# Performance work log

Hardware: AMD Instinct MI355X
Metric: run time of the kernel (lower is better)

Reference implementation:

```python
import jax, jax.numpy as jnp
import numpy as np

N = 50000          # nodes
E = 800000         # edges per metapath
M = 3              # metapaths
IN_DIM = 256
H = 8              # heads
D = 32             # out_dim per head
HID = 128          # semantic attention hidden
NEG_SLOPE = 0.2    # DGL GATConv default leaky_relu slope


def setup_inputs() -> dict:
    key = jax.random.key(0)
    ks = jax.random.split(key, 10)
    h = jax.random.normal(ks[0], (N, IN_DIM), dtype=jnp.float32)
    src = jax.random.randint(ks[1], (M, E), 0, N, dtype=jnp.int32)
    dst = jax.random.randint(ks[2], (M, E), 0, N, dtype=jnp.int32)
    s = 1.0 / np.sqrt(IN_DIM)
    fc_w = jax.random.normal(ks[3], (M, IN_DIM, H * D), dtype=jnp.float32) * s
    attn_l = jax.random.normal(ks[4], (M, H, D), dtype=jnp.float32) * 0.1
    attn_r = jax.random.normal(ks[5], (M, H, D), dtype=jnp.float32) * 0.1
    bias = jnp.zeros((M, H * D), dtype=jnp.float32)
    sem_w1 = jax.random.normal(ks[6], (H * D, HID), dtype=jnp.float32) * (1.0 / np.sqrt(H * D))
    sem_b1 = jnp.zeros((HID,), dtype=jnp.float32)
    sem_w2 = jax.random.normal(ks[7], (HID, 1), dtype=jnp.float32) * (1.0 / np.sqrt(HID))
    return {"h": h, "src": src, "dst": dst, "fc_w": fc_w, "attn_l": attn_l,
            "attn_r": attn_r, "bias": bias, "sem_w1": sem_w1, "sem_b1": sem_b1,
            "sem_w2": sem_w2}


def _gat(h, src, dst, fc_w, attn_l, attn_r, bias):
    # DGL GATConv (eval mode, dropout=0), activation=elu.
    feat = (h @ fc_w).reshape(N, H, D)                       # [N,H,D]
    el = jnp.sum(feat * attn_l, axis=-1)                     # [N,H]
    er = jnp.sum(feat * attn_r, axis=-1)                     # [N,H]
    e = jax.nn.leaky_relu(el[src] + er[dst], NEG_SLOPE)      # [E,H]
    # edge softmax over incoming edges of each dst node
    emax = jax.ops.segment_max(e, dst, num_segments=N)       # [N,H]
    emax = jnp.where(jnp.isfinite(emax), emax, 0.0)
    ee = jnp.exp(e - emax[dst])                              # [E,H]
    esum = jax.ops.segment_sum(ee, dst, num_segments=N)      # [N,H]
    alpha = ee / jnp.maximum(esum[dst], 1e-38)               # [E,H]
    msg = feat[src] * alpha[:, :, None]                      # [E,H,D]
    rst = jax.ops.segment_sum(msg, dst, num_segments=N)      # [N,H,D]
    rst = rst + bias.reshape(1, H, D)
    return jax.nn.elu(rst).reshape(N, H * D)                 # flatten heads


def reference(h, src, dst, fc_w, attn_l, attn_r, bias, sem_w1, sem_b1, sem_w2):
    gat_all = jax.vmap(_gat, in_axes=(None, 0, 0, 0, 0, 0, 0))
    z_m = gat_all(h, src, dst, fc_w, attn_l, attn_r, bias)   # [M,N,F]
    z_m = jnp.transpose(z_m, (1, 0, 2))                      # [N,M,F]
    # semantic attention
    w = jnp.tanh(z_m @ sem_w1 + sem_b1) @ sem_w2             # [N,M,1]
    w = w.mean(axis=0)                                       # [M,1]
    a_w = jax.nn.softmax(w, axis=0)                          # [M,1]
    z = jnp.sum(z_m * a_w[None, :, :], axis=1)               # [N,F]
    return z
```

## Files before the change

kernel.cpp:

```cpp
#include <hip/hip_runtime.h>
#include <math.h>

#define NN   50000
#define EE   800000
#define MM   3
#define KDIM 256
#define FF   256
#define HH   8
#define DD   32
#define HID  128
#define SLOPE 0.2f
#define BK   32
#define CAP  80

typedef unsigned short u16;
typedef unsigned int   u32;
typedef __attribute__((ext_vector_type(8))) short short8;
typedef __attribute__((ext_vector_type(4))) float floatx4;

__device__ __forceinline__ float eluf(float x) { return x > 0.f ? x : expm1f(x); }

__device__ __forceinline__ float b2f_lo(u32 u) {
    union { u32 i; float f; } v; v.i = u << 16; return v.f;
}
__device__ __forceinline__ float b2f_hi(u32 u) {
    union { u32 i; float f; } v; v.i = u & 0xffff0000u; return v.f;
}
__device__ __forceinline__ u16 f2b(float f) {
    union { float f; u32 i; } v; v.f = f;
    u32 lsb = (v.i >> 16) & 1u;
    v.i += 0x7fffu + lsb;
    return (u16)(v.i >> 16);
}
__device__ __forceinline__ u32 pack2(float lo, float hi) {
    return (u32)f2b(lo) | ((u32)f2b(hi) << 16);
}

__device__ __forceinline__ void gload_lds16(const u16* g, u16* l) {
    __builtin_amdgcn_global_load_lds(
        (const __attribute__((address_space(1))) unsigned int*)(const void*)g,
        (__attribute__((address_space(3))) unsigned int*)(void*)l,
        16, 0, 0);
}

__global__ __launch_bounds__(256) void k_cast_h(
    const float* __restrict__ hmat, u16* __restrict__ hb)
{
    long long i = ((long long)blockIdx.x * 256 + threadIdx.x) * 8;
    if (i >= (long long)NN * KDIM) return;
    float4 v0 = *(const float4*)(hmat + i);
    float4 v1 = *(const float4*)(hmat + i + 4);
    uint4 u;
    u.x = pack2(v0.x, v0.y); u.y = pack2(v0.z, v0.w);
    u.z = pack2(v1.x, v1.y); u.w = pack2(v1.z, v1.w);
    *(uint4*)(hb + i) = u;
}

__global__ __launch_bounds__(256) void k_cast_w(
    const float* __restrict__ fcw, u16* __restrict__ fcwt)
{
    int k = blockIdx.x, m = blockIdx.y, n = threadIdx.x;
    float v = fcw[((size_t)m * KDIM + k) * FF + n];
    fcwt[((size_t)m * FF + n) * KDIM + k] = f2b(v);
}

__global__ __launch_bounds__(128) void k_cast_w1(
    const float* __restrict__ w1, u16* __restrict__ w1t)
{
    int k = blockIdx.x, n = threadIdx.x;
    w1t[(size_t)n * KDIM + k] = f2b(w1[(size_t)k * HID + n]);
}

__global__ __launch_bounds__(256) void k_feat_all(
    const u16*   __restrict__ hb,
    const u16*   __restrict__ fcwt,
    const float* __restrict__ al,
    const float* __restrict__ ar,
    u16*   __restrict__ featb,
    float* __restrict__ el,
    float* __restrict__ er,
    const int* __restrict__ src,
    const int* __restrict__ dst,
    int* __restrict__ cnt,
    u16* __restrict__ srt)
{
    __shared__ u16 As[128 * BK];
    __shared__ u16 Bs[128 * BK];

    const int t = threadIdx.x;

    {
        int bid = blockIdx.x + 391 * (blockIdx.y + 2 * blockIdx.z);
        long long base = ((long long)bid * 256 + t) * 4;
        if (base < (long long)MM * EE) {
            int4 d4 = *(const int4*)(dst + base);
            int4 s4 = *(const int4*)(src + base);
            int me = (int)(base / EE);
            int* cnt_m = cnt + (size_t)me * NN;
            u16* srt_m = srt + (size_t)me * CAP * NN;
            int dd4[4] = { d4.x, d4.y, d4.z, d4.w };
            int ss4[4] = { s4.x, s4.y, s4.z, s4.w };
            #pragma unroll
            for (int j = 0; j < 4; ++j) {
                int slot = atomicAdd(&cnt_m[dd4[j]], 1);
                if (slot < CAP) srt_m[(size_t)slot * NN + dd4[j]] = (u16)ss4[j];
            }
        }
    }

    const int n0 = blockIdx.x * 128;
    const int cy = blockIdx.y;
    const int m  = blockIdx.z;
    const int c_base = cy * 128;
    const int wave = t >> 6, lane = t & 63;
    const int wr = wave >> 1, wc = wave & 1;
    const int quad = lane >> 4, l15 = lane & 15;

    const u16* fcwt_m = fcwt + (size_t)m * FF * KDIM;
    const float* al_m = al + (size_t)m * HH * DD;
    const float* ar_m = ar + (size_t)m * HH * DD;

    const u16* pA[2]; const u16* pB[2]; u16* lA[2]; u16* lB[2];
    #pragma unroll
    for (int i = 0; i < 2; ++i) {
        int r  = wave * 32 + i * 16 + (lane >> 2);
        int cs = (((lane & 3) ^ (r & 3)) << 3);
        pA[i] = hb + (size_t)min(n0 + r, NN - 1) * KDIM + cs;
        pB[i] = fcwt_m + (size_t)(c_base + r) * KDIM + cs;
        lA[i] = (u16*)As + (wave * 2 + i) * 512;
        lB[i] = (u16*)Bs + (wave * 2 + i) * 512;
    }

    int aoff[4], boff[4];
    #pragma unroll
    for (int ti = 0; ti < 4; ++ti) {
        int rowa = wr * 64 + ti * 16 + l15;
        aoff[ti] = rowa * BK + (((quad ^ (rowa & 3))) << 3);
        int rowb = wc * 64 + ti * 16 + l15;
        boff[ti] = rowb * BK + (((quad ^ (rowb & 3))) << 3);
    }

    floatx4 acc[4][4] = {};

    for (int k0 = 0; k0 < KDIM; k0 += BK) {
        __syncthreads();
        #pragma unroll
        for (int i = 0; i < 2; ++i) {
            gload_lds16(pA[i] + k0, lA[i]);
            gload_lds16(pB[i] + k0, lB[i]);
        }
        __syncthreads();

        short8 afr[4], bfr[4];
        #pragma unroll
        for (int ti = 0; ti < 4; ++ti)
            afr[ti] = *(const short8*)(&As[aoff[ti]]);
        #pragma unroll
        for (int tj = 0; tj < 4; ++tj)
            bfr[tj] = *(const short8*)(&Bs[boff[tj]]);
        #pragma unroll
        for (int ti = 0; ti < 4; ++ti)
            #pragma unroll
            for (int tj = 0; tj < 4; ++tj)
                acc[ti][tj] = __builtin_amdgcn_mfma_f32_16x16x32_bf16(
                    afr[ti], bfr[tj], acc[ti][tj], 0, 0, 0);
    }

    float alv[4], arv[4];
    #pragma unroll
    for (int tj = 0; tj < 4; ++tj) {
        int h = cy * 4 + wc * 2 + (tj >> 1);
        int dcol = (tj & 1) * 16 + l15;
        alv[tj] = al_m[h * DD + dcol];
        arv[tj] = ar_m[h * DD + dcol];
    }
    const int h0 = cy * 4 + wc * 2, h1 = h0 + 1;

    #pragma unroll
    for (int ti = 0; ti < 4; ++ti) {
        #pragma unroll
        for (int reg = 0; reg < 4; ++reg) {
            int n = n0 + wr * 64 + ti * 16 + quad * 4 + reg;
            bool ok = n < NN;
            if (ok) {
                #pragma unroll
                for (int tj = 0; tj < 4; ++tj) {
                    int c = c_base + wc * 64 + tj * 16 + l15;
                    featb[((size_t)m * NN + n) * FF + c] = f2b(acc[ti][tj][reg]);
                }
            }
            float pl0 = acc[ti][0][reg] * alv[0] + acc[ti][1][reg] * alv[1];
            float pl1 = acc[ti][2][reg] * alv[2] + acc[ti][3][reg] * alv[3];
            float pr0 = acc[ti][0][reg] * arv[0] + acc[ti][1][reg] * arv[1];
            float pr1 = acc[ti][2][reg] * arv[2] + acc[ti][3][reg] * arv[3];
            #pragma unroll
            for (int s = 1; s < 16; s <<= 1) {
                pl0 += __shfl_xor(pl0, s); pl1 += __shfl_xor(pl1, s);
                pr0 += __shfl_xor(pr0, s); pr1 += __shfl_xor(pr1, s);
            }
            if (l15 == 0 && ok) {
                el[((size_t)m * NN + n) * HH + h0] = pl0;
                el[((size_t)m * NN + n) * HH + h1] = pl1;
                er[((size_t)m * NN + n) * HH + h0] = pr0;
                er[((size_t)m * NN + n) * HH + h1] = pr1;
            }
        }
    }
}

__global__ __launch_bounds__(256) void k_aggr_all(
    const int* __restrict__ cnt,
    const u16* __restrict__ srt,
    const float* __restrict__ el,
    const float* __restrict__ er,
    const u16* __restrict__ featb,
    const float* __restrict__ bias,
    u16* __restrict__ z,
    int m)
{
    __shared__ float alpha_s[4][2][CAP][HH];
    __shared__ int   srcoff[4][2][CAP];

    const int wave = threadIdx.x >> 6, lane = threadIdx.x & 63;
    const int half = lane >> 5, L = lane & 31;
    const int d = blockIdx.x * 8 + wave * 2 + half;

    const int deg = min(cnt[(size_t)m * NN + d], CAP);
    const float* el_m = el + (size_t)m * NN * HH;
    const u16* feat_m = featb + (size_t)m * NN * FF;

    #pragma unroll
    for (int i = 0; i < 3; ++i) {
        int slot = L + i * 32;
        if (slot < deg)
            srcoff[wave][half][slot] =
                (int)srt[(size_t)(m * CAP + slot) * NN + d] * FF;
    }

    const int hA = L & 7;
    const float er_d = er[((size_t)m * NN + d) * HH + hA];
    float esum_r = 0.f;
    const int nIter = (deg + 3) >> 2;
    int i = 0;
    for (; i + 2 <= nIter; i += 2) {
        int j0 = i * 4 + (L >> 3);
        int j1 = j0 + 4;
        bool v0 = j0 < deg, v1 = j1 < deg;
        int so0 = v0 ? srcoff[wave][half][j0] : 0;
        int so1 = v1 ? srcoff[wave][half][j1] : 0;
        float x0 = el_m[(size_t)(so0 >> 5) + hA] + er_d;
        float x1 = el_m[(size_t)(so1 >> 5) + hA] + er_d;
        x0 = x0 >= 0.f ? x0 : SLOPE * x0;  x0 = fminf(x0, 60.f);
        x1 = x1 >= 0.f ? x1 : SLOPE * x1;  x1 = fminf(x1, 60.f);
        float e0 = v0 ? expf(x0) : 0.f;
        float e1 = v1 ? expf(x1) : 0.f;
        if (v0) alpha_s[wave][half][j0][hA] = e0;
        if (v1) alpha_s[wave][half][j1][hA] = e1;
        float g = e0 + e1;
        g += __shfl_xor(g, 8); g += __shfl_xor(g, 16);
        esum_r += g;
    }
    for (; i < nIter; ++i) {
        int j = i * 4 + (L >> 3);
        float e = 0.f;
        if (j < deg) {
            int so = srcoff[wave][half][j];
            float x = el_m[(size_t)(so >> 5) + hA] + er_d;
            x = x >= 0.f ? x : SLOPE * x;
            x = fminf(x, 60.f);
            e = expf(x);
            alpha_s[wave][half][j][hA] = e;
        }
        float g = e;
        g += __shfl_xor(g, 8); g += __shfl_xor(g, 16);
        esum_r += g;
    }
    float inv_r = 1.f / fmaxf(esum_r, 1e-38f);

    const float inv_g = __shfl(inv_r, (lane & 32) | (L >> 2));
    const int hB = L >> 2;
    const u16* frow = feat_m + L * 8;
    float acc[8] = {0.f, 0.f, 0.f, 0.f, 0.f, 0.f, 0.f, 0.f};

#define ACC8(f, a)                                                  \
    acc[0] += (a) * b2f_lo((f).x); acc[1] += (a) * b2f_hi((f).x);   \
    acc[2] += (a) * b2f_lo((f).y); acc[3] += (a) * b2f_hi((f).y);   \
    acc[4] += (a) * b2f_lo((f).z); acc[5] += (a) * b2f_hi((f).z);   \
    acc[6] += (a) * b2f_lo((f).w); acc[7] += (a) * b2f_hi((f).w);

    int j = 0;
    for (; j + 4 <= deg; j += 4) {
        int so0 = srcoff[wave][half][j + 0];
        int so1 = srcoff[wave][half][j + 1];
        int so2 = srcoff[wave][half][j + 2];
        int so3 = srcoff[wave][half][j + 3];
        float a0 = alpha_s[wave][half][j + 0][hB];
        float a1 = alpha_s[wave][half][j + 1][hB];
        float a2 = alpha_s[wave][half][j + 2][hB];
        float a3 = alpha_s[wave][half][j + 3][hB];
        uint4 f0 = *(const uint4*)(frow + so0);
        uint4 f1 = *(const uint4*)(frow + so1);
        uint4 f2 = *(const uint4*)(frow + so2);
        uint4 f3 = *(const uint4*)(frow + so3);
        ACC8(f0, a0); ACC8(f1, a1); ACC8(f2, a2); ACC8(f3, a3);
    }
    for (; j < deg; ++j) {
        int so = srcoff[wave][half][j];
        float a = alpha_s[wave][half][j][hB];
        uint4 f = *(const uint4*)(frow + so);
        ACC8(f, a);
    }
#undef ACC8

    #pragma unroll
    for (int k = 0; k < 8; ++k) acc[k] *= inv_g;

    const float4 b0 = *(const float4*)(bias + (size_t)m * FF + L * 8);
    const float4 b1 = *(const float4*)(bias + (size_t)m * FF + L * 8 + 4);
    uint4 o;
    o.x = pack2(eluf(acc[0] + b0.x), eluf(acc[1] + b0.y));
    o.y = pack2(eluf(acc[2] + b0.z), eluf(acc[3] + b0.w));
    o.z = pack2(eluf(acc[4] + b1.x), eluf(acc[5] + b1.y));
    o.w = pack2(eluf(acc[6] + b1.z), eluf(acc[7] + b1.w));
    *(uint4*)(z + ((size_t)m * NN + d) * FF + L * 8) = o;
}

__global__ __launch_bounds__(256) void k_sem_all(
    const u16* __restrict__ z,
    const u16* __restrict__ w1t,
    const float* __restrict__ b1,
    const float* __restrict__ w2,
    float* __restrict__ wsum)
{
    __shared__ u16 As[128 * BK];
    __shared__ u16 Bs[128 * BK];

    const int n0 = blockIdx.x * 128;
    const int m  = blockIdx.y;
    const int t = threadIdx.x;
    const int wave = t >> 6, lane = t & 63;
    const int wr = wave >> 1, wc = wave & 1;
    const int quad = lane >> 4, l15 = lane & 15;

    const u16* z_m = z + (size_t)m * NN * FF;

    const u16* pA[2]; const u16* pB[2]; u16* lA[2]; u16* lB[2];
    #pragma unroll
    for (int i = 0; i < 2; ++i) {
        int r  = wave * 32 + i * 16 + (lane >> 2);
        int cs = (((lane & 3) ^ (r & 3)) << 3);
        pA[i] = z_m + (size_t)min(n0 + r, NN - 1) * FF + cs;
        pB[i] = w1t + (size_t)r * KDIM + cs;
        lA[i] = (u16*)As + (wave * 2 + i) * 512;
        lB[i] = (u16*)Bs + (wave * 2 + i) * 512;
    }

    int aoff[4], boff[4];
    #pragma unroll
    for (int ti = 0; ti < 4; ++ti) {
        int rowa = wr * 64 + ti * 16 + l15;
        aoff[ti] = rowa * BK + (((quad ^ (rowa & 3))) << 3);
        int rowb = wc * 64 + ti * 16 + l15;
        boff[ti] = rowb * BK + (((quad ^ (rowb & 3))) << 3);
    }

    floatx4 acc[4][4] = {};

    for (int k0 = 0; k0 < KDIM; k0 += BK) {
        __syncthreads();
        #pragma unroll
        for (int i = 0; i < 2; ++i) {
            gload_lds16(pA[i] + k0, lA[i]);
            gload_lds16(pB[i] + k0, lB[i]);
        }
        __syncthreads();

        short8 afr[4], bfr[4];
        #pragma unroll
        for (int ti = 0; ti < 4; ++ti)
            afr[ti] = *(const short8*)(&As[aoff[ti]]);
        #pragma unroll
        for (int tj = 0; tj < 4; ++tj)
            bfr[tj] = *(const short8*)(&Bs[boff[tj]]);
        #pragma unroll
        for (int ti = 0; ti < 4; ++ti)
            #pragma unroll
            for (int tj = 0; tj < 4; ++tj)
                acc[ti][tj] = __builtin_amdgcn_mfma_f32_16x16x32_bf16(
                    afr[ti], bfr[tj], acc[ti][tj], 0, 0, 0);
    }

    float b1v[4], w2v[4];
    #pragma unroll
    for (int tj = 0; tj < 4; ++tj) {
        int c = wc * 64 + tj * 16 + l15;
        b1v[tj] = b1[c];
        w2v[tj] = w2[c];
    }
    float local = 0.f;
    #pragma unroll
    for (int ti = 0; ti < 4; ++ti) {
        #pragma unroll
        for (int reg = 0; reg < 4; ++reg) {
            int n = n0 + wr * 64 + ti * 16 + quad * 4 + reg;
            if (n < NN) {
                #pragma unroll
                for (int tj = 0; tj < 4; ++tj)
                    local += tanhf(acc[ti][tj][reg] + b1v[tj]) * w2v[tj];
            }
        }
    }
    #pragma unroll
    for (int s = 1; s < 64; s <<= 1) local += __shfl_xor(local, s);
    if (lane == 0) atomicAdd(&wsum[m], local);
}

__global__ __launch_bounds__(256) void k_combine(
    const u16* __restrict__ z, const float* __restrict__ wsum,
    float* __restrict__ out)
{
    float s0 = wsum[0] / (float)NN, s1 = wsum[1] / (float)NN, s2 = wsum[2] / (float)NN;
    float mx = fmaxf(s0, fmaxf(s1, s2));
    float e0 = expf(s0 - mx), e1 = expf(s1 - mx), e2 = expf(s2 - mx);
    float inv = 1.f / (e0 + e1 + e2);
    float aw[3] = { e0 * inv, e1 * inv, e2 * inv };

    long long idx = (long long)blockIdx.x * 256 + threadIdx.x;
    if (idx >= (long long)NN * 32) return;
    int n = (int)(idx >> 5), c = (int)(idx & 31) * 8;
    float acc[8] = {0.f, 0.f, 0.f, 0.f, 0.f, 0.f, 0.f, 0.f};
    #pragma unroll
    for (int m = 0; m < MM; ++m) {
        uint4 f = *(const uint4*)(z + ((size_t)m * NN + n) * FF + c);
        float a = aw[m];
        acc[0] += a * b2f_lo(f.x); acc[1] += a * b2f_hi(f.x);
        acc[2] += a * b2f_lo(f.y); acc[3] += a * b2f_hi(f.y);
        acc[4] += a * b2f_lo(f.z); acc[5] += a * b2f_hi(f.z);
        acc[6] += a * b2f_lo(f.w); acc[7] += a * b2f_hi(f.w);
    }
    float* op = out + (size_t)n * FF + c;
    *(float4*)op       = make_float4(acc[0], acc[1], acc[2], acc[3]);
    *(float4*)(op + 4) = make_float4(acc[4], acc[5], acc[6], acc[7]);
}

extern "C" void kernel_launch(void* const* d_in, const int* in_sizes, int n_in,
                              void* d_out, int out_size, void* d_ws, size_t ws_size,
                              hipStream_t stream)
{
    const float* hmat = (const float*)d_in[0];
    const int*   src  = (const int*)d_in[1];
    const int*   dst  = (const int*)d_in[2];
    const float* fcw  = (const float*)d_in[3];
    const float* al   = (const float*)d_in[4];
    const float* ar   = (const float*)d_in[5];
    const float* bias = (const float*)d_in[6];
    const float* w1   = (const float*)d_in[7];
    const float* b1   = (const float*)d_in[8];
    const float* w2   = (const float*)d_in[9];
    float* out = (float*)d_out;

    char* ws = (char*)d_ws;
    size_t off = 0;
    auto alloc = [&](size_t nbytes) {
        void* p = (void*)(ws + off);
        off = (off + nbytes + 255) & ~(size_t)255;
        return p;
    };
    float* el   = (float*)alloc((size_t)MM * NN * HH * 4);
    float* er   = (float*)alloc((size_t)MM * NN * HH * 4);
    float* wsum = (float*)alloc(256);
    int*   cnt  = (int*)alloc((size_t)MM * NN * 4);
    u16*   srt  = (u16*)alloc((size_t)MM * CAP * NN * 2);
    u16*   fcwt = (u16*)alloc((size_t)MM * KDIM * FF * 2);
    u16*   w1t  = (u16*)alloc((size_t)HID * KDIM * 2);
    u16*   hb   = (u16*)alloc((size_t)NN * KDIM * 2);
    u16*   featb= (u16*)alloc((size_t)MM * NN * FF * 2);
    u16*   z    = (u16*)alloc((size_t)MM * NN * FF * 2);

    hipMemsetAsync(wsum, 0, 256, stream);
    hipMemsetAsync(cnt, 0, (size_t)MM * NN * 4, stream);

    k_cast_h<<<(int)(((size_t)NN * KDIM / 8 + 255) / 256), 256, 0, stream>>>(hmat, hb);
    k_cast_w<<<dim3(KDIM, MM), 256, 0, stream>>>(fcw, fcwt);
    k_cast_w1<<<KDIM, 128, 0, stream>>>(w1, w1t);

    k_feat_all<<<dim3((NN + 127) / 128, 2, MM), 256, 0, stream>>>(
        hb, fcwt, al, ar, featb, el, er, src, dst, cnt, srt);

    for (int m = 0; m < MM; ++m)
        k_aggr_all<<<NN / 8, 256, 0, stream>>>(
            cnt, srt, el, er, featb, bias, z, m);

    k_sem_all<<<dim3((NN + 127) / 128, MM), 256, 0, stream>>>(z, w1t, b1, w2, wsum);
    k_combine<<<(int)(((size_t)NN * 32 + 255) / 256), 256, 0, stream>>>(z, wsum, out);
}
```

Before: 569.2 us.

## Merge cast kernels with partial edge scatter; split feat and sem per metapath

The three cast kernels become one k_prep launch, which also scatters the first part of each metapath's edges into the per-destination buckets. The remaining edges are scattered inside per-metapath k_feat launches. The semantic GEMM is now launched per metapath right after that metapath's aggregation, so z for that metapath may still be in cache. This cuts launch count for the casts and spreads the atomic scatter work differently across kernels, at the cost of more launches for feat and sem, each with a smaller grid.

```diff
diff --git a/kernel.cpp b/kernel.cpp
--- a/kernel.cpp
+++ b/kernel.cpp
@@ -13,6 +13,15 @@
 #define BK   32
 #define CAP  80
 
+#define EPREP_BLK 272
+#define E_OFF     (EPREP_BLK * 1024)
+#define E_REST    (EE - E_OFF)
+#define PREP_SCAT (EPREP_BLK * MM)
+#define PREP_CH   6250
+#define PREP_CW   768
+#define PREP_CW1  128
+#define PREP_GRID (PREP_SCAT + PREP_CH + PREP_CW + PREP_CW1)
+
 typedef unsigned short u16;
 typedef unsigned int   u32;
 typedef __attribute__((ext_vector_type(8))) short short8;
@@ -43,35 +52,67 @@
         16, 0, 0);
 }
 
-__global__ __launch_bounds__(256) void k_cast_h(
-    const float* __restrict__ hmat, u16* __restrict__ hb)
-{
-    long long i = ((long long)blockIdx.x * 256 + threadIdx.x) * 8;
-    if (i >= (long long)NN * KDIM) return;
-    float4 v0 = *(const float4*)(hmat + i);
-    float4 v1 = *(const float4*)(hmat + i + 4);
-    uint4 u;
-    u.x = pack2(v0.x, v0.y); u.y = pack2(v0.z, v0.w);
-    u.z = pack2(v1.x, v1.y); u.w = pack2(v1.z, v1.w);
-    *(uint4*)(hb + i) = u;
-}
-
-__global__ __launch_bounds__(256) void k_cast_w(
-    const float* __restrict__ fcw, u16* __restrict__ fcwt)
-{
-    int k = blockIdx.x, m = blockIdx.y, n = threadIdx.x;
-    float v = fcw[((size_t)m * KDIM + k) * FF + n];
-    fcwt[((size_t)m * FF + n) * KDIM + k] = f2b(v);
-}
-
-__global__ __launch_bounds__(128) void k_cast_w1(
-    const float* __restrict__ w1, u16* __restrict__ w1t)
-{
-    int k = blockIdx.x, n = threadIdx.x;
-    w1t[(size_t)n * KDIM + k] = f2b(w1[(size_t)k * HID + n]);
-}
-
-__global__ __launch_bounds__(256) void k_feat_all(
+__device__ __forceinline__ void scat4(
+    const int* __restrict__ src, const int* __restrict__ dst,
+    int* __restrict__ cnt, u16* __restrict__ srt, int me, long long base)
+{
+    int4 d4 = *(const int4*)(dst + base);
+    int4 s4 = *(const int4*)(src + base);
+    int* cnt_m = cnt + (size_t)me * NN;
+    u16* srt_m = srt + (size_t)me * CAP * NN;
+    int dd4[4] = { d4.x, d4.y, d4.z, d4.w };
+    int ss4[4] = { s4.x, s4.y, s4.z, s4.w };
+    #pragma unroll
+    for (int j = 0; j < 4; ++j) {
+        int slot = atomicAdd(&cnt_m[dd4[j]], 1);
+        if (slot < CAP) srt_m[(size_t)slot * NN + dd4[j]] = (u16)ss4[j];
+    }
+}
+
+__global__ __launch_bounds__(256) void k_prep(
+    const float* __restrict__ hmat, u16* __restrict__ hb,
+    const float* __restrict__ fcw,  u16* __restrict__ fcwt,
+    const float* __restrict__ w1,   u16* __restrict__ w1t,
+    const int* __restrict__ src, const int* __restrict__ dst,
+    int* __restrict__ cnt, u16* __restrict__ srt)
+{
+    const int bid = blockIdx.x;
+    const int t = threadIdx.x;
+
+    if (bid < PREP_SCAT) {
+        int me = bid / EPREP_BLK, c = bid % EPREP_BLK;
+        long long base = (long long)me * EE + ((long long)c * 256 + t) * 4;
+        scat4(src, dst, cnt, srt, me, base);
+        return;
+    }
+    if (bid < PREP_SCAT + PREP_CH) {
+        long long i = (((long long)(bid - PREP_SCAT)) * 256 + t) * 8;
+        if (i < (long long)NN * KDIM) {
+            float4 v0 = *(const float4*)(hmat + i);
+            float4 v1 = *(const float4*)(hmat + i + 4);
+            uint4 u;
+            u.x = pack2(v0.x, v0.y); u.y = pack2(v0.z, v0.w);
+            u.z = pack2(v1.x, v1.y); u.w = pack2(v1.z, v1.w);
+            *(uint4*)(hb + i) = u;
+        }
+        return;
+    }
+    if (bid < PREP_SCAT + PREP_CH + PREP_CW) {
+        int wb = bid - PREP_SCAT - PREP_CH;
+        int k = wb & 255, me = wb >> 8, n = t;
+        float v = fcw[((size_t)me * KDIM + k) * FF + n];
+        fcwt[((size_t)me * FF + n) * KDIM + k] = f2b(v);
+        return;
+    }
+    {
+        int vb = bid - PREP_SCAT - PREP_CH - PREP_CW;
+        int idx = vb * 256 + t;
+        int k = idx >> 7, n = idx & 127;
+        w1t[(size_t)n * KDIM + k] = f2b(w1[(size_t)k * HID + n]);
+    }
+}
+
+__global__ __launch_bounds__(256) void k_feat(
     const u16*   __restrict__ hb,
     const u16*   __restrict__ fcwt,
     const float* __restrict__ al,
@@ -82,7 +123,8 @@
     const int* __restrict__ src,
     const int* __restrict__ dst,
     int* __restrict__ cnt,
-    u16* __restrict__ srt)
+    u16* __restrict__ srt,
+    int m)
 {
     __shared__ u16 As[128 * BK];
     __shared__ u16 Bs[128 * BK];
@@ -90,27 +132,14 @@
     const int t = threadIdx.x;
 
     {
-        int bid = blockIdx.x + 391 * (blockIdx.y + 2 * blockIdx.z);
-        long long base = ((long long)bid * 256 + t) * 4;
-        if (base < (long long)MM * EE) {
-            int4 d4 = *(const int4*)(dst + base);
-            int4 s4 = *(const int4*)(src + base);
-            int me = (int)(base / EE);
-            int* cnt_m = cnt + (size_t)me * NN;
-            u16* srt_m = srt + (size_t)me * CAP * NN;
-            int dd4[4] = { d4.x, d4.y, d4.z, d4.w };
-            int ss4[4] = { s4.x, s4.y, s4.z, s4.w };
-            #pragma unroll
-            for (int j = 0; j < 4; ++j) {
-                int slot = atomicAdd(&cnt_m[dd4[j]], 1);
-                if (slot < CAP) srt_m[(size_t)slot * NN + dd4[j]] = (u16)ss4[j];
-            }
-        }
+        int bf = blockIdx.x + 391 * blockIdx.y;
+        long long off = ((long long)bf * 256 + t) * 4;
+        if (off < E_REST)
+            scat4(src, dst, cnt, srt, m, (long long)m * EE + E_OFF + off);
     }
 
     const int n0 = blockIdx.x * 128;
     const int cy = blockIdx.y;
-    const int m  = blockIdx.z;
     const int c_base = cy * 128;
     const int wave = t >> 6, lane = t & 63;
     const int wr = wave >> 1, wc = wave & 1;
@@ -330,13 +359,13 @@
     const u16* __restrict__ w1t,
     const float* __restrict__ b1,
     const float* __restrict__ w2,
-    float* __restrict__ wsum)
+    float* __restrict__ wsum,
+    int m)
 {
     __shared__ u16 As[128 * BK];
     __shared__ u16 Bs[128 * BK];
 
     const int n0 = blockIdx.x * 128;
-    const int m  = blockIdx.y;
     const int t = threadIdx.x;
     const int wave = t >> 6, lane = t & 63;
     const int wr = wave >> 1, wc = wave & 1;
@@ -480,17 +509,18 @@
     hipMemsetAsync(wsum, 0, 256, stream);
     hipMemsetAsync(cnt, 0, (size_t)MM * NN * 4, stream);
 
-    k_cast_h<<<(int)(((size_t)NN * KDIM / 8 + 255) / 256), 256, 0, stream>>>(hmat, hb);
-    k_cast_w<<<dim3(KDIM, MM), 256, 0, stream>>>(fcw, fcwt);
-    k_cast_w1<<<KDIM, 128, 0, stream>>>(w1, w1t);
-
-    k_feat_all<<<dim3((NN + 127) / 128, 2, MM), 256, 0, stream>>>(
-        hb, fcwt, al, ar, featb, el, er, src, dst, cnt, srt);
+    k_prep<<<PREP_GRID, 256, 0, stream>>>(
+        hmat, hb, fcw, fcwt, w1, w1t, src, dst, cnt, srt);
 
     for (int m = 0; m < MM; ++m)
+        k_feat<<<dim3(391, 2), 256, 0, stream>>>(
+            hb, fcwt, al, ar, featb, el, er, src, dst, cnt, srt, m);
+
+    for (int m = 0; m < MM; ++m) {
         k_aggr_all<<<NN / 8, 256, 0, stream>>>(
             cnt, srt, el, er, featb, bias, z, m);
-
-    k_sem_all<<<dim3((NN + 127) / 128, MM), 256, 0, stream>>>(z, w1t, b1, w2, wsum);
+        k_sem_all<<<391, 256, 0, stream>>>(z, w1t, b1, w2, wsum, m);
+    }
+
     k_combine<<<(int)(((size_t)NN * 32 + 255) / 256), 256, 0, stream>>>(z, wsum, out);
 }
```

Result: slower. 635.3 us (+11.6%).

## Fuse h cast into GEMM loads, merge weight casts and per-metapath aggregation launches

Applied to the files above, without the earlier changes.

Removes the separate fp32-to-bf16 cast kernel for h: the GEMM now reads fp32 rows directly, converts them in registers and writes them to LDS, so the bf16 copy of h is never written to or read back from global memory. The two weight-cast kernels are merged into one launch, and the three per-metapath aggregation launches become a single 2D grid. In exchange, the A-tile load becomes a synchronous register round-trip instead of an async global-to-LDS load. h is also re-read and re-converted in fp32 by every column block and metapath (6 times).

```diff
diff --git a/kernel.cpp b/kernel.cpp
--- a/kernel.cpp
+++ b/kernel.cpp
@@ -43,36 +43,24 @@
         16, 0, 0);
 }
 
-__global__ __launch_bounds__(256) void k_cast_h(
-    const float* __restrict__ hmat, u16* __restrict__ hb)
-{
-    long long i = ((long long)blockIdx.x * 256 + threadIdx.x) * 8;
-    if (i >= (long long)NN * KDIM) return;
-    float4 v0 = *(const float4*)(hmat + i);
-    float4 v1 = *(const float4*)(hmat + i + 4);
-    uint4 u;
-    u.x = pack2(v0.x, v0.y); u.y = pack2(v0.z, v0.w);
-    u.z = pack2(v1.x, v1.y); u.w = pack2(v1.z, v1.w);
-    *(uint4*)(hb + i) = u;
-}
-
-__global__ __launch_bounds__(256) void k_cast_w(
-    const float* __restrict__ fcw, u16* __restrict__ fcwt)
-{
-    int k = blockIdx.x, m = blockIdx.y, n = threadIdx.x;
-    float v = fcw[((size_t)m * KDIM + k) * FF + n];
-    fcwt[((size_t)m * FF + n) * KDIM + k] = f2b(v);
-}
-
-__global__ __launch_bounds__(128) void k_cast_w1(
-    const float* __restrict__ w1, u16* __restrict__ w1t)
-{
-    int k = blockIdx.x, n = threadIdx.x;
-    w1t[(size_t)n * KDIM + k] = f2b(w1[(size_t)k * HID + n]);
+__global__ __launch_bounds__(256) void k_prep_w(
+    const float* __restrict__ fcw,  u16* __restrict__ fcwt,
+    const float* __restrict__ w1,   u16* __restrict__ w1t)
+{
+    const int bid = blockIdx.x;
+    if (bid < 768) {
+        int k = bid & 255, me = bid >> 8, n = threadIdx.x;
+        float v = fcw[((size_t)me * KDIM + k) * FF + n];
+        fcwt[((size_t)me * FF + n) * KDIM + k] = f2b(v);
+    } else {
+        int idx = (bid - 768) * 256 + threadIdx.x;
+        int k = idx >> 7, n = idx & 127;
+        w1t[(size_t)n * KDIM + k] = f2b(w1[(size_t)k * HID + n]);
+    }
 }
 
 __global__ __launch_bounds__(256) void k_feat_all(
-    const u16*   __restrict__ hb,
+    const float* __restrict__ hmat,
     const u16*   __restrict__ fcwt,
     const float* __restrict__ al,
     const float* __restrict__ ar,
@@ -120,14 +108,14 @@
     const float* al_m = al + (size_t)m * HH * DD;
     const float* ar_m = ar + (size_t)m * HH * DD;
 
-    const u16* pA[2]; const u16* pB[2]; u16* lA[2]; u16* lB[2];
+    const float* pAf[2]; const u16* pB[2]; u16* lA[2]; u16* lB[2];
     #pragma unroll
     for (int i = 0; i < 2; ++i) {
         int r  = wave * 32 + i * 16 + (lane >> 2);
         int cs = (((lane & 3) ^ (r & 3)) << 3);
-        pA[i] = hb + (size_t)min(n0 + r, NN - 1) * KDIM + cs;
-        pB[i] = fcwt_m + (size_t)(c_base + r) * KDIM + cs;
-        lA[i] = (u16*)As + (wave * 2 + i) * 512;
+        pAf[i] = hmat + (size_t)min(n0 + r, NN - 1) * KDIM + cs;
+        pB[i]  = fcwt_m + (size_t)(c_base + r) * KDIM + cs;
+        lA[i] = (u16*)As + (wave * 2 + i) * 512 + lane * 8;
         lB[i] = (u16*)Bs + (wave * 2 + i) * 512;
     }
 
@@ -145,9 +133,16 @@
     for (int k0 = 0; k0 < KDIM; k0 += BK) {
         __syncthreads();
         #pragma unroll
+        for (int i = 0; i < 2; ++i)
+            gload_lds16(pB[i] + k0, lB[i]);
+        #pragma unroll
         for (int i = 0; i < 2; ++i) {
-            gload_lds16(pA[i] + k0, lA[i]);
-            gload_lds16(pB[i] + k0, lB[i]);
+            float4 v0 = *(const float4*)(pAf[i] + k0);
+            float4 v1 = *(const float4*)(pAf[i] + k0 + 4);
+            uint4 u;
+            u.x = pack2(v0.x, v0.y); u.y = pack2(v0.z, v0.w);
+            u.z = pack2(v1.x, v1.y); u.w = pack2(v1.z, v1.w);
+            *(uint4*)(lA[i]) = u;
         }
         __syncthreads();
 
@@ -215,12 +210,12 @@
     const float* __restrict__ er,
     const u16* __restrict__ featb,
     const float* __restrict__ bias,
-    u16* __restrict__ z,
-    int m)
+    u16* __restrict__ z)
 {
     __shared__ float alpha_s[4][2][CAP][HH];
     __shared__ int   srcoff[4][2][CAP];
 
+    const int m = blockIdx.y;
     const int wave = threadIdx.x >> 6, lane = threadIdx.x & 63;
     const int half = lane >> 5, L = lane & 31;
     const int d = blockIdx.x * 8 + wave * 2 + half;
@@ -473,24 +468,19 @@
     u16*   srt  = (u16*)alloc((size_t)MM * CAP * NN * 2);
     u16*   fcwt = (u16*)alloc((size_t)MM * KDIM * FF * 2);
     u16*   w1t  = (u16*)alloc((size_t)HID * KDIM * 2);
-    u16*   hb   = (u16*)alloc((size_t)NN * KDIM * 2);
     u16*   featb= (u16*)alloc((size_t)MM * NN * FF * 2);
     u16*   z    = (u16*)alloc((size_t)MM * NN * FF * 2);
 
     hipMemsetAsync(wsum, 0, 256, stream);
     hipMemsetAsync(cnt, 0, (size_t)MM * NN * 4, stream);
 
-    k_cast_h<<<(int)(((size_t)NN * KDIM / 8 + 255) / 256), 256, 0, stream>>>(hmat, hb);
-    k_cast_w<<<dim3(KDIM, MM), 256, 0, stream>>>(fcw, fcwt);
-    k_cast_w1<<<KDIM, 128, 0, stream>>>(w1, w1t);
+    k_prep_w<<<896, 256, 0, stream>>>(fcw, fcwt, w1, w1t);
 
     k_feat_all<<<dim3((NN + 127) / 128, 2, MM), 256, 0, stream>>>(
-        hb, fcwt, al, ar, featb, el, er, src, dst, cnt, srt);
-
-    for (int m = 0; m < MM; ++m)
-        k_aggr_all<<<NN / 8, 256, 0, stream>>>(
-            cnt, srt, el, er, featb, bias, z, m);
-
+        hmat, fcwt, al, ar, featb, el, er, src, dst, cnt, srt);
+
+    k_aggr_all<<<dim3(NN / 8, MM), 256, 0, stream>>>(
+        cnt, srt, el, er, featb, bias, z);
     k_sem_all<<<dim3((NN + 127) / 128, MM), 256, 0, stream>>>(z, w1t, b1, w2, wsum);
     k_combine<<<(int)(((size_t)NN * 32 + 255) / 256), 256, 0, stream>>>(z, wsum, out);
 }
```

After: 557.9 us. -2.0%, faster.
